# Kernel optimization log

Measured on AMD Instinct MI355X. Metric: run time of the kernel, lower is better.

## Reference

```python
import jax, jax.numpy as jnp
import numpy as np


def setup_inputs() -> dict:
    key = jax.random.key(0)
    k1, k2 = jax.random.split(key)
    inp = jax.random.normal(k1, (16, 64, 64, 64), dtype=jnp.float32)  # (B, D, H, W)
    codebook = jax.random.normal(k2, (1024, 64), dtype=jnp.float32)  # (K, D)
    return {"input": inp, "codebook": codebook}


def reference(input, codebook):
    # input: (B, D, *spatial); codebook: (K, D)
    B, D = input.shape[0], input.shape[1]
    spatial = input.shape[2:]
    # move channel dim last, flatten to tokens: (N, D)
    x = jnp.moveaxis(input, 1, -1).reshape(-1, D)
    # squared L2 distances (cdist^2), computed via expansion to avoid (N,K,D)
    x_sq = jnp.sum(x * x, axis=-1, keepdims=True)            # (N, 1)
    e_sq = jnp.sum(codebook * codebook, axis=-1)             # (K,)
    dist = x_sq - 2.0 * (x @ codebook.T) + e_sq              # (N, K)
    idx = jnp.argmin(dist, axis=-1)                          # (N,)
    quantized = jnp.take(codebook, idx, axis=0)              # (N, D)
    # reshape back to (B, *spatial, D) then move D to axis 1
    out = jnp.moveaxis(quantized.reshape((B,) + spatial + (D,)), -1, 1)
    indices = idx.reshape((B,) + spatial)
    return out, indices
```

## Files before the change

### kernel.cpp

```cpp
#include <hip/hip_runtime.h>


typedef _Float16 v8h  __attribute__((ext_vector_type(8)));
typedef _Float16 v4h  __attribute__((ext_vector_type(4)));
typedef float    v16f __attribute__((ext_vector_type(16)));

constexpr int   D         = 64;
constexpr int   K         = 1024;
constexpr int   HW        = 4096;
constexpr int   DHW       = D * HW;
constexpr int   OUT_ELEMS = 16 * DHW;
constexpr float EPS       = 2e-3f;

__global__ __launch_bounds__(512, 2) void vq_fused(
    const float* __restrict__ input,
    const float* __restrict__ codebook,
    float* __restrict__ out)
{
    __shared__ _Float16 s_ch[8][2][4][64][8];
    __shared__ _Float16 s_bf[8][2][4][64][8];
    __shared__ float    s_esq[K];
    __shared__ int      s_idx[256];
    __shared__ int      s_list[256];
    __shared__ int      s_cnt;
    __shared__ float    s_xf[64];
    __shared__ float    s_redv[8];
    __shared__ int      s_redk[8];

    const int tid  = threadIdx.x;
    const int lane = tid & 63;
    const int q    = __builtin_amdgcn_readfirstlane(tid >> 6);
    const int lh   = lane >> 5;
    const int tok0 = blockIdx.x * 256;
    const int b    = tok0 >> 12;
    const int hwb  = tok0 & 4095;

    if (tid == 0) s_cnt = 0;

    {
        const float* xb = input + (size_t)b * DHW + hwb;
        #pragma unroll
        for (int pass = 0; pass < 8; ++pass) {
            const int g   = pass * 512 + tid;
            const int d   = g >> 6;
            const int hw4 = (g & 63) * 4;
            const float4 v = *(const float4*)(xb + (size_t)d * HW + hw4);
            const float vv[4] = {v.x, v.y, v.z, v.w};
            const int kc = d >> 4, lhd = (d >> 3) & 1, j = d & 7;
            #pragma unroll
            for (int u = 0; u < 4; ++u) {
                const int tk  = hw4 + u;
                const int g2  = tk >> 5, col = tk & 31;
                const float f = vv[u];
                const _Float16 fh = (_Float16)f;
                s_bf[g2][0][kc][lhd * 32 + col][j] = fh;
                s_bf[g2][1][kc][lhd * 32 + col][j] = (_Float16)(f - (float)fh);
            }
        }
    }

    v8h b5 = {};
    if (lh == 0) { b5[0] = (_Float16)1.0f; b5[1] = (_Float16)1.0f; }

    v8h bh[4], bl[4];
    v16f Z = {0,0,0,0,0,0,0,0,0,0,0,0,0,0,0,0};
    const float INF = __builtin_huge_valf();
    float bv = INF, b2 = INF;
    int   sl = 0;
    bool  bloaded = false;

    #pragma unroll 1
    for (int p = 0; p < 4; ++p) {
        const int phR = (blockIdx.x + p) & 3;
        const int cw0 = phR * 256;

        #pragma unroll
        for (int pass = 0; pass < 8; ++pass) {
            const int g   = pass * 512 + tid;
            const int cwl = g >> 4;
            const int dq  = (g & 15) * 4;
            const float4 v = *(const float4*)(codebook + (size_t)(cw0 + cwl) * D + dq);
            float part = fmaf(v.x, v.x, fmaf(v.y, v.y, fmaf(v.z, v.z, v.w * v.w)));
            part += __shfl_xor(part, 1, 64);
            part += __shfl_xor(part, 2, 64);
            part += __shfl_xor(part, 4, 64);
            part += __shfl_xor(part, 8, 64);
            if ((tid & 15) == 0) s_esq[cw0 + cwl] = part;
            const int T  = cwl >> 5, lc = cwl & 31;
            const int kc = dq >> 4, lhd = (dq >> 3) & 1, j0 = dq & 7;
            const float vv[4] = {v.x, v.y, v.z, v.w};
            v4h hh, hl;
            #pragma unroll
            for (int u = 0; u < 4; ++u) {
                const float w = -2.0f * vv[u];
                const _Float16 wh = (_Float16)w;
                hh[u] = wh;
                hl[u] = (_Float16)(w - (float)wh);
            }
            *(v4h*)&s_ch[T][0][kc][lhd * 32 + lc][j0] = hh;
            *(v4h*)&s_ch[T][1][kc][lhd * 32 + lc][j0] = hl;
        }
        __syncthreads();

        if (!bloaded) {
            bloaded = true;
            #pragma unroll
            for (int kc = 0; kc < 4; ++kc) {
                bh[kc] = *(const v8h*)&s_bf[q][0][kc][lane][0];
                bl[kc] = *(const v8h*)&s_bf[q][1][kc][lane][0];
            }
        }

        #pragma unroll 1
        for (int t = 0; t < 8; ++t) {
            const int Tg = phR * 8 + t;
            float e = 0.0f;
            if (lane < 32) e = s_esq[cw0 + t * 32 + lane];
            v8h ae = {};
            const _Float16 eh = (_Float16)e;
            ae[0] = eh;
            ae[1] = (_Float16)(e - (float)eh);

            const v8h ah0 = *(const v8h*)&s_ch[t][0][0][lane][0];
            const v8h ah1 = *(const v8h*)&s_ch[t][0][1][lane][0];
            const v8h ah2 = *(const v8h*)&s_ch[t][0][2][lane][0];
            const v8h ah3 = *(const v8h*)&s_ch[t][0][3][lane][0];
            const v8h al0 = *(const v8h*)&s_ch[t][1][0][lane][0];
            const v8h al1 = *(const v8h*)&s_ch[t][1][1][lane][0];
            const v8h al2 = *(const v8h*)&s_ch[t][1][2][lane][0];
            const v8h al3 = *(const v8h*)&s_ch[t][1][3][lane][0];

            v16f accA = __builtin_amdgcn_mfma_f32_32x32x16_f16(ae,  b5,    Z,    0, 0, 0);
            v16f accB = __builtin_amdgcn_mfma_f32_32x32x16_f16(al0, bh[0], Z,    0, 0, 0);
            accA = __builtin_amdgcn_mfma_f32_32x32x16_f16(ah0, bh[0], accA, 0, 0, 0);
            accB = __builtin_amdgcn_mfma_f32_32x32x16_f16(al1, bh[1], accB, 0, 0, 0);
            accA = __builtin_amdgcn_mfma_f32_32x32x16_f16(ah1, bh[1], accA, 0, 0, 0);
            accB = __builtin_amdgcn_mfma_f32_32x32x16_f16(al2, bh[2], accB, 0, 0, 0);
            accA = __builtin_amdgcn_mfma_f32_32x32x16_f16(ah2, bh[2], accA, 0, 0, 0);
            accB = __builtin_amdgcn_mfma_f32_32x32x16_f16(al3, bh[3], accB, 0, 0, 0);
            accA = __builtin_amdgcn_mfma_f32_32x32x16_f16(ah3, bh[3], accA, 0, 0, 0);
            accB = __builtin_amdgcn_mfma_f32_32x32x16_f16(ah0, bl[0], accB, 0, 0, 0);
            accB = __builtin_amdgcn_mfma_f32_32x32x16_f16(ah1, bl[1], accB, 0, 0, 0);
            accB = __builtin_amdgcn_mfma_f32_32x32x16_f16(ah2, bl[2], accB, 0, 0, 0);
            accB = __builtin_amdgcn_mfma_f32_32x32x16_f16(ah3, bl[3], accB, 0, 0, 0);

            #pragma unroll
            for (int r = 0; r < 16; ++r) {
                const float s = accA[r] + accB[r];
                b2 = __builtin_amdgcn_fmed3f(s, bv, b2);
                if (s < bv) { bv = s; sl = (Tg << 4) | r; }
            }
        }
        __syncthreads();
    }

    {
        const float obv = __shfl_xor(bv, 32, 64);
        const float ob2 = __shfl_xor(b2, 32, 64);
        const int   osl = __shfl_xor(sl, 32, 64);
        const bool  oth = obv < bv;
        const float B1  = oth ? obv : bv;
        const float B2  = fminf(fmaxf(bv, obv), fminf(b2, ob2));
        const int   wsl = oth ? osl : sl;
        const int   wlh = oth ? (lh ^ 1) : lh;
        const int   r   = wsl & 15;
        const int   Tt  = wsl >> 4;
        const int   cw  = Tt * 32 + (r & 3) + 8 * (r >> 2) + 4 * wlh;
        if (lane < 32) {
            s_idx[q * 32 + lane] = cw;
            if (B2 - B1 < EPS) {
                const int pos = atomicAdd(&s_cnt, 1);
                s_list[pos] = q * 32 + lane;
            }
        }
    }
    __syncthreads();

    {
        const int cnt = s_cnt;
        const int rr  = tid >> 3;
        const int c   = tid & 7;
        for (int ii = 0; ii < cnt; ++ii) {
            const int tl = s_list[ii];
            if (tid < 64)
                s_xf[tid] = input[(size_t)b * DHW + (size_t)tid * HW + (hwb + tl)];
            __syncthreads();
            const float4* xs4 = (const float4*)&s_xf[c * 8];
            const float4 x0 = xs4[0], x1 = xs4[1];
            float bestv = INF; int bestk = K;
            #pragma unroll 4
            for (int i = 0; i < 16; ++i) {
                const int k = i * 64 + rr;
                const float4* c4 = (const float4*)(codebook + (size_t)k * D + c * 8);
                const float4 c0 = c4[0], c1 = c4[1];
                float p0 = 0.f, p1 = 0.f;
                p0 = fmaf(x0.x, c0.x, p0); p0 = fmaf(x0.y, c0.y, p0);
                p0 = fmaf(x0.z, c0.z, p0); p0 = fmaf(x0.w, c0.w, p0);
                p1 = fmaf(x1.x, c1.x, p1); p1 = fmaf(x1.y, c1.y, p1);
                p1 = fmaf(x1.z, c1.z, p1); p1 = fmaf(x1.w, c1.w, p1);
                float dp = p0 + p1;
                dp += __shfl_xor(dp, 1, 64);
                dp += __shfl_xor(dp, 2, 64);
                dp += __shfl_xor(dp, 4, 64);
                const float s = fmaf(-2.0f, dp, s_esq[k]);
                if (s < bestv) { bestv = s; bestk = k; }
            }
            #pragma unroll
            for (int off = 8; off <= 32; off <<= 1) {
                const float ov = __shfl_xor(bestv, off, 64);
                const int   ok = __shfl_xor(bestk, off, 64);
                if (ov < bestv || (ov == bestv && ok < bestk)) { bestv = ov; bestk = ok; }
            }
            if (lane == 0) { s_redv[q] = bestv; s_redk[q] = bestk; }
            __syncthreads();
            if (tid == 0) {
                float bb = s_redv[0]; int bk = s_redk[0];
                #pragma unroll
                for (int w = 1; w < 8; ++w) {
                    const float v = s_redv[w]; const int kk = s_redk[w];
                    if (v < bb || (v == bb && kk < bk)) { bb = v; bk = kk; }
                }
                s_idx[tl] = bk;
            }
            __syncthreads();
        }
    }

    {
        const int token = tid & 255;
        const int dh    = tid >> 8;
        const int idx   = s_idx[token];
        const float4* c4 = (const float4*)(codebook + (size_t)idx * D + dh * 32);
        float4 cr[8];
        #pragma unroll
        for (int j = 0; j < 8; ++j) cr[j] = c4[j];
        float* ob = out + (size_t)b * DHW + (size_t)dh * 32 * HW + hwb + token;
        #pragma unroll
        for (int j = 0; j < 8; ++j) {
            ob[(size_t)(4 * j + 0) * HW] = cr[j].x;
            ob[(size_t)(4 * j + 1) * HW] = cr[j].y;
            ob[(size_t)(4 * j + 2) * HW] = cr[j].z;
            ob[(size_t)(4 * j + 3) * HW] = cr[j].w;
        }
        if (tid < 256) out[OUT_ELEMS + tok0 + tid] = (float)s_idx[tid];
    }
}

extern "C" void kernel_launch(void* const* d_in, const int* in_sizes, int n_in,
                              void* d_out, int out_size, void* d_ws, size_t ws_size,
                              hipStream_t stream) {
    const float* input    = (const float*)d_in[0];
    const float* codebook = (const float*)d_in[1];
    float* out            = (float*)d_out;
    vq_fused<<<256, 512, 0, stream>>>(input, codebook, out);
}
```

Measured before the change: 117.4 us.

## Stage raw fp32 input in LDS and restructure codebook staging and norm precompute

The input tile is now kept in shared memory as raw fp32. Each lane builds its own hi/lo fp16 operand registers from that copy, and the fallback exact recheck also reads it instead of going back to global memory. All codebook squared norms are computed once up front in a separate pass, rather than folded into each phase's staging. The per-phase codebook staging now has each thread write a full 8-wide fp16 vector per row chunk, which removes the scattered 2-byte LDS writes and narrower stores. In exchange the kernel uses more shared memory (a 64x260 float buffer), which may limit occupancy, and the codebook is read from global one extra time for the norms.

```diff
diff --git a/kernel.cpp b/kernel.cpp
--- a/kernel.cpp
+++ b/kernel.cpp
@@ -2,7 +2,6 @@
 
 
 typedef _Float16 v8h  __attribute__((ext_vector_type(8)));
-typedef _Float16 v4h  __attribute__((ext_vector_type(4)));
 typedef float    v16f __attribute__((ext_vector_type(16)));
 
 constexpr int   D         = 64;
@@ -11,6 +10,7 @@
 constexpr int   DHW       = D * HW;
 constexpr int   OUT_ELEMS = 16 * DHW;
 constexpr float EPS       = 2e-3f;
+constexpr int   RAWS      = 260;
 
 __global__ __launch_bounds__(512, 2) void vq_fused(
     const float* __restrict__ input,
@@ -18,7 +18,7 @@
     float* __restrict__ out)
 {
     __shared__ _Float16 s_ch[8][2][4][64][8];
-    __shared__ _Float16 s_bf[8][2][4][64][8];
+    __shared__ float    s_raw[64][RAWS];
     __shared__ float    s_esq[K];
     __shared__ int      s_idx[256];
     __shared__ int      s_list[256];
@@ -44,30 +44,46 @@
             const int g   = pass * 512 + tid;
             const int d   = g >> 6;
             const int hw4 = (g & 63) * 4;
-            const float4 v = *(const float4*)(xb + (size_t)d * HW + hw4);
-            const float vv[4] = {v.x, v.y, v.z, v.w};
-            const int kc = d >> 4, lhd = (d >> 3) & 1, j = d & 7;
-            #pragma unroll
-            for (int u = 0; u < 4; ++u) {
-                const int tk  = hw4 + u;
-                const int g2  = tk >> 5, col = tk & 31;
-                const float f = vv[u];
+            *(float4*)&s_raw[d][hw4] = *(const float4*)(xb + (size_t)d * HW + hw4);
+        }
+    }
+
+    #pragma unroll 4
+    for (int p = 0; p < 32; ++p) {
+        const int g  = p * 512 + tid;
+        const int cw = g >> 4;
+        const int dq = (g & 15) * 4;
+        const float4 v = *(const float4*)(codebook + (size_t)cw * D + dq);
+        float part = fmaf(v.x, v.x, fmaf(v.y, v.y, fmaf(v.z, v.z, v.w * v.w)));
+        part += __shfl_xor(part, 1, 64);
+        part += __shfl_xor(part, 2, 64);
+        part += __shfl_xor(part, 4, 64);
+        part += __shfl_xor(part, 8, 64);
+        if ((tid & 15) == 0) s_esq[cw] = part;
+    }
+    __syncthreads();
+
+    v8h bh[4], bl[4];
+    {
+        const int tok = q * 32 + (lane & 31);
+        #pragma unroll
+        for (int kc = 0; kc < 4; ++kc)
+            #pragma unroll
+            for (int j = 0; j < 8; ++j) {
+                const float f = s_raw[kc * 16 + lh * 8 + j][tok];
                 const _Float16 fh = (_Float16)f;
-                s_bf[g2][0][kc][lhd * 32 + col][j] = fh;
-                s_bf[g2][1][kc][lhd * 32 + col][j] = (_Float16)(f - (float)fh);
-            }
-        }
+                bh[kc][j] = fh;
+                bl[kc][j] = (_Float16)(f - (float)fh);
+            }
     }
 
     v8h b5 = {};
     if (lh == 0) { b5[0] = (_Float16)1.0f; b5[1] = (_Float16)1.0f; }
 
-    v8h bh[4], bl[4];
     v16f Z = {0,0,0,0,0,0,0,0,0,0,0,0,0,0,0,0};
     const float INF = __builtin_huge_valf();
     float bv = INF, b2 = INF;
     int   sl = 0;
-    bool  bloaded = false;
 
     #pragma unroll 1
     for (int p = 0; p < 4; ++p) {
@@ -75,41 +91,28 @@
         const int cw0 = phR * 256;
 
         #pragma unroll
-        for (int pass = 0; pass < 8; ++pass) {
-            const int g   = pass * 512 + tid;
-            const int cwl = g >> 4;
-            const int dq  = (g & 15) * 4;
-            const float4 v = *(const float4*)(codebook + (size_t)(cw0 + cwl) * D + dq);
-            float part = fmaf(v.x, v.x, fmaf(v.y, v.y, fmaf(v.z, v.z, v.w * v.w)));
-            part += __shfl_xor(part, 1, 64);
-            part += __shfl_xor(part, 2, 64);
-            part += __shfl_xor(part, 4, 64);
-            part += __shfl_xor(part, 8, 64);
-            if ((tid & 15) == 0) s_esq[cw0 + cwl] = part;
-            const int T  = cwl >> 5, lc = cwl & 31;
-            const int kc = dq >> 4, lhd = (dq >> 3) & 1, j0 = dq & 7;
-            const float vv[4] = {v.x, v.y, v.z, v.w};
-            v4h hh, hl;
-            #pragma unroll
-            for (int u = 0; u < 4; ++u) {
-                const float w = -2.0f * vv[u];
+        for (int pass = 0; pass < 4; ++pass) {
+            const int F  = pass * 512 + tid;
+            const int r  = F & 63;
+            const int kc = (F >> 6) & 3;
+            const int Tl = F >> 8;
+            const int cw = cw0 + Tl * 32 + (r & 31);
+            const int d0 = kc * 16 + (r >> 5) * 8;
+            const float4 u0 = *(const float4*)(codebook + (size_t)cw * D + d0);
+            const float4 u1 = *(const float4*)(codebook + (size_t)cw * D + d0 + 4);
+            const float vv[8] = {u0.x, u0.y, u0.z, u0.w, u1.x, u1.y, u1.z, u1.w};
+            v8h hh, hl;
+            #pragma unroll
+            for (int j = 0; j < 8; ++j) {
+                const float w = -2.0f * vv[j];
                 const _Float16 wh = (_Float16)w;
-                hh[u] = wh;
-                hl[u] = (_Float16)(w - (float)wh);
-            }
-            *(v4h*)&s_ch[T][0][kc][lhd * 32 + lc][j0] = hh;
-            *(v4h*)&s_ch[T][1][kc][lhd * 32 + lc][j0] = hl;
+                hh[j] = wh;
+                hl[j] = (_Float16)(w - (float)wh);
+            }
+            *(v8h*)&s_ch[Tl][0][kc][r][0] = hh;
+            *(v8h*)&s_ch[Tl][1][kc][r][0] = hl;
         }
         __syncthreads();
-
-        if (!bloaded) {
-            bloaded = true;
-            #pragma unroll
-            for (int kc = 0; kc < 4; ++kc) {
-                bh[kc] = *(const v8h*)&s_bf[q][0][kc][lane][0];
-                bl[kc] = *(const v8h*)&s_bf[q][1][kc][lane][0];
-            }
-        }
 
         #pragma unroll 1
         for (int t = 0; t < 8; ++t) {
@@ -182,8 +185,7 @@
         const int c   = tid & 7;
         for (int ii = 0; ii < cnt; ++ii) {
             const int tl = s_list[ii];
-            if (tid < 64)
-                s_xf[tid] = input[(size_t)b * DHW + (size_t)tid * HW + (hwb + tl)];
+            if (tid < 64) s_xf[tid] = s_raw[tid][tl];
             __syncthreads();
             const float4* xs4 = (const float4*)&s_xf[c * 8];
             const float4 x0 = xs4[0], x1 = xs4[1];
```

After: 118.0 us. No clear change (+0.6%).
